# Performance work log

Measured on AMD Instinct MI355X. Metric: run time of the kernel, lower is better.

The kernel has to match this reference:

```python
import jax, jax.numpy as jnp
import numpy as np

N_LEVELS = 20
F = 2                      # n_features_per_level
LOG2T = 19
T = 1 << LOG2T             # hashmap size per level
BASE_RES = 16
PER_LEVEL_SCALE = 1.39
N_POINTS = 1_000_000

# 8 corner offsets of a voxel, (8, 3)
OFFSETS = np.array([[i, j, k] for i in (0, 1) for j in (0, 1) for k in (0, 1)], dtype=np.int32)
# spatial hash primes (only 3 needed for 3D input); uint32 multiply wraps like torch int32 bits
PRIME_Y = np.uint32(2654435761)
PRIME_Z = np.uint32(805459861)


def setup_inputs() -> dict:
    key = jax.random.key(0)
    k1, k2 = jax.random.split(key)
    x = jax.random.uniform(k1, (N_POINTS, 3), dtype=jnp.float32)  # points in [0,1)^3
    # nn.init.uniform_(weight, a=-1e-4, b=1e-4), one table per level, stacked
    tables = jax.random.uniform(k2, (N_LEVELS, T, F), minval=-1e-4, maxval=1e-4, dtype=jnp.float32)
    return {"x": x, "tables": tables}


def _hash(coords):
    # coords: (..., 3) int32 voxel corner indices -> (...,) int32 in [0, T)
    c = coords.astype(jnp.uint32)
    h = c[..., 0] ^ (c[..., 1] * PRIME_Y) ^ (c[..., 2] * PRIME_Z)
    return (h & jnp.uint32(T - 1)).astype(jnp.int32)


def _encode_level(x, table, resolution):
    xs = x * resolution                      # (B, 3)
    vmin = jnp.floor(xs).astype(jnp.int32)   # (B, 3)
    corners = vmin[:, None, :] + OFFSETS[None, :, :]   # (B, 8, 3)
    idx = _hash(corners)                     # (B, 8)
    e = table[idx]                           # (B, 8, F) gather
    w = xs - vmin                            # fractional position, (B, 3)
    wx, wy, wz = w[:, 0:1], w[:, 1:2], w[:, 2:3]
    # trilinear interpolation, exact lerp chain from the torch module
    c00 = e[:, 0] * (1 - wx) + e[:, 4] * wx
    c01 = e[:, 1] * (1 - wx) + e[:, 5] * wx
    c10 = e[:, 2] * (1 - wx) + e[:, 6] * wx
    c11 = e[:, 3] * (1 - wx) + e[:, 7] * wx
    c0 = c00 * (1 - wy) + c10 * wy
    c1 = c01 * (1 - wy) + c11 * wy
    return c0 * (1 - wz) + c1 * wz           # (B, F)


def reference(x, tables):
    outs = [_encode_level(x, tables[i], int(BASE_RES * PER_LEVEL_SCALE ** i))
            for i in range(N_LEVELS)]
    return jnp.concatenate(outs, axis=-1)    # (B, N_LEVELS * F) = (B, 40)
```

## Files before the change

kernel.cpp:

```cpp
#include <hip/hip_runtime.h>
#include <hip/hip_fp16.h>

#define NLEV 20
#define TSIZE (1u << 19)
#define TMASK (TSIZE - 1u)
#define PRIME_Y 2654435761u
#define PRIME_Z 805459861u

typedef float f32x2 __attribute__((ext_vector_type(2)));
typedef float f32x4 __attribute__((ext_vector_type(4)));

__device__ __constant__ int kRes[NLEV] = {
    16, 22, 30, 42, 59, 83, 115, 160, 222, 309,
    430, 598, 832, 1156, 1608, 2235, 3107, 4318, 6003, 8344};

__device__ __forceinline__ float2 encode_one(const float2* __restrict__ tbl,
                                             float r, float px, float py,
                                             float pz) {
  const float xs0 = px * r, xs1 = py * r, xs2 = pz * r;
  const float f0 = floorf(xs0), f1 = floorf(xs1), f2 = floorf(xs2);
  const float wx = xs0 - f0, wy = xs1 - f1, wz = xs2 - f2;
  const unsigned v0 = (unsigned)(int)f0;
  const unsigned v1 = (unsigned)(int)f1;
  const unsigned v2 = (unsigned)(int)f2;

  const unsigned hy0 = v1 * PRIME_Y, hy1 = (v1 + 1u) * PRIME_Y;
  const unsigned hz0 = v2 * PRIME_Z, hz1 = (v2 + 1u) * PRIME_Z;
  unsigned H[4];
  H[0] = hy0 ^ hz0;
  H[1] = hy0 ^ hz1;
  H[2] = hy1 ^ hz0;
  H[3] = hy1 ^ hz1;

  float2 e0[4], e1[4];

  if ((v0 & 1u) == 0u) {
#pragma unroll
    for (int j = 0; j < 4; ++j) {
      const unsigned i0 = (v0 ^ H[j]) & TMASK;
      const f32x4 q = *(const f32x4*)((const float*)tbl + 2u * (i0 & ~1u));
      const bool lo = (i0 & 1u) == 0u;
      e0[j] = lo ? make_float2(q.x, q.y) : make_float2(q.z, q.w);
      e1[j] = lo ? make_float2(q.z, q.w) : make_float2(q.x, q.y);
    }
  } else {
#pragma unroll
    for (int j = 0; j < 4; ++j) {
      e0[j] = tbl[(v0 ^ H[j]) & TMASK];
      e1[j] = tbl[((v0 + 1u) ^ H[j]) & TMASK];
    }
  }

  const float owx = 1.0f - wx, owy = 1.0f - wy, owz = 1.0f - wz;

  const float c00a = e0[0].x * owx + e1[0].x * wx;
  const float c01a = e0[1].x * owx + e1[1].x * wx;
  const float c10a = e0[2].x * owx + e1[2].x * wx;
  const float c11a = e0[3].x * owx + e1[3].x * wx;
  const float c0a = c00a * owy + c10a * wy;
  const float c1a = c01a * owy + c11a * wy;

  const float c00b = e0[0].y * owx + e1[0].y * wx;
  const float c01b = e0[1].y * owx + e1[1].y * wx;
  const float c10b = e0[2].y * owx + e1[2].y * wx;
  const float c11b = e0[3].y * owx + e1[3].y * wx;
  const float c0b = c00b * owy + c10b * wy;
  const float c1b = c01b * owy + c11b * wy;

  return make_float2(c0a * owz + c1a * wz, c0b * owz + c1b * wz);
}

__global__ __launch_bounds__(256) void enc_level_kernel(
    const float* __restrict__ x, const float* __restrict__ tables,
    unsigned* __restrict__ ws16, int n) {
  const int l = blockIdx.y;
  const int p = blockIdx.x * 256 + threadIdx.x;
  if (p >= n) return;
  const float px = __builtin_nontemporal_load(x + 3 * p + 0);
  const float py = __builtin_nontemporal_load(x + 3 * p + 1);
  const float pz = __builtin_nontemporal_load(x + 3 * p + 2);
  const float2* __restrict__ tbl = (const float2*)tables + (size_t)l * TSIZE;
  const float2 v = encode_one(tbl, (float)kRes[l], px, py, pz);
  const __half2 h = __floats2half2_rn(v.x, v.y);
  __builtin_nontemporal_store(*(const unsigned*)&h, ws16 + (size_t)l * n + p);
}

__global__ __launch_bounds__(256) void transpose_kernel(
    const unsigned* __restrict__ ws16, float* __restrict__ out, int n) {
  __shared__ unsigned lds[128 * 21];
  const int p0 = blockIdx.x * 128;
  const int t = threadIdx.x;
  const int npts = min(128, n - p0);

#pragma unroll
  for (int k = 0; k < 10; ++k) {
    const int g = t + k * 256;
    const int l = g >> 7;
    const int pl = g & 127;
    if (pl < npts) {
      lds[pl * 21 + l] =
          __builtin_nontemporal_load(ws16 + (size_t)l * n + p0 + pl);
    }
  }
  __syncthreads();

  f32x4* __restrict__ dst = (f32x4*)(out + (size_t)p0 * (NLEV * 2));
#pragma unroll
  for (int k = 0; k < 5; ++k) {
    const int g = t + k * 256;
    const int pl = g / 10;
    const int comp = g - pl * 10;
    if (pl < npts) {
      const unsigned u0 = lds[pl * 21 + comp * 2 + 0];
      const unsigned u1 = lds[pl * 21 + comp * 2 + 1];
      const float2 a = __half22float2(*(const __half2*)&u0);
      const float2 b = __half22float2(*(const __half2*)&u1);
      f32x4 v;
      v.x = a.x;
      v.y = a.y;
      v.z = b.x;
      v.w = b.y;
      __builtin_nontemporal_store(v, dst + g);
    }
  }
}

__global__ __launch_bounds__(256) void hash_enc_kernel(
    const float* __restrict__ x, const float* __restrict__ tables,
    float* __restrict__ out, int n) {
  int p = blockIdx.x * 256 + threadIdx.x;
  if (p >= n) return;
  const float px = x[3 * p + 0];
  const float py = x[3 * p + 1];
  const float pz = x[3 * p + 2];
  float o[NLEV * 2];
#pragma unroll
  for (int l = 0; l < NLEV; ++l) {
    const float2* tbl = (const float2*)tables + (size_t)l * TSIZE;
    const float2 v = encode_one(tbl, (float)kRes[l], px, py, pz);
    o[2 * l + 0] = v.x;
    o[2 * l + 1] = v.y;
  }
  float4* __restrict__ dst = (float4*)(out + (size_t)p * (NLEV * 2));
#pragma unroll
  for (int k = 0; k < 10; ++k) {
    dst[k] = make_float4(o[4 * k + 0], o[4 * k + 1], o[4 * k + 2], o[4 * k + 3]);
  }
}

extern "C" void kernel_launch(void* const* d_in, const int* in_sizes, int n_in,
                              void* d_out, int out_size, void* d_ws, size_t ws_size,
                              hipStream_t stream) {
  const float* x = (const float*)d_in[0];
  const float* tables = (const float*)d_in[1];
  float* out = (float*)d_out;
  const int n = in_sizes[0] / 3;
  const size_t ws_needed = (size_t)NLEV * n * sizeof(unsigned);

  if (ws_size >= ws_needed) {
    const int pblocks = (n + 255) / 256;
    dim3 grid1(pblocks, NLEV);
    enc_level_kernel<<<grid1, 256, 0, stream>>>(x, tables, (unsigned*)d_ws, n);
    const int tblocks = (n + 127) / 128;
    transpose_kernel<<<tblocks, 256, 0, stream>>>((const unsigned*)d_ws, out, n);
  } else {
    const int grid = (n + 255) / 256;
    hash_enc_kernel<<<grid, 256, 0, stream>>>(x, tables, out, n);
  }
}
```

Baseline: 653.7 us.

## Fuse fine hash-grid levels into a per-point kernel, keep coarse levels staged

Coarse levels 0-9 still run as a per-level grid that writes fp16 results to a workspace, which a smaller transpose kernel then scatters into the output. Fine levels 10-19 are computed by a new per-point kernel that loops over those levels and writes fp32 results directly into the upper half of each output row. This cuts workspace traffic and transpose work in half. The trade-off is that gathers across the large fine tables are interleaved per point rather than done one table at a time, which may reduce cache locality.

```diff
diff --git a/kernel.cpp b/kernel.cpp
--- a/kernel.cpp
+++ b/kernel.cpp
@@ -85,20 +85,51 @@
   __builtin_nontemporal_store(*(const unsigned*)&h, ws16 + (size_t)l * n + p);
 }
 
+__global__ __launch_bounds__(256) void fused_fine_kernel(
+    const float* __restrict__ x, const float* __restrict__ tables,
+    float* __restrict__ out, int n) {
+  const int p = blockIdx.x * 256 + threadIdx.x;
+  if (p >= n) return;
+  const float px = __builtin_nontemporal_load(x + 3 * p + 0);
+  const float py = __builtin_nontemporal_load(x + 3 * p + 1);
+  const float pz = __builtin_nontemporal_load(x + 3 * p + 2);
+
+  float o[20];
+#pragma unroll
+  for (int li = 0; li < 10; ++li) {
+    const int l = 10 + li;
+    const float2* __restrict__ tbl = (const float2*)tables + (size_t)l * TSIZE;
+    const float2 v = encode_one(tbl, (float)kRes[l], px, py, pz);
+    o[2 * li + 0] = v.x;
+    o[2 * li + 1] = v.y;
+  }
+
+  float* __restrict__ dstf = out + (size_t)p * (NLEV * 2) + 20;
+#pragma unroll
+  for (int k = 0; k < 5; ++k) {
+    f32x4 v;
+    v.x = o[4 * k + 0];
+    v.y = o[4 * k + 1];
+    v.z = o[4 * k + 2];
+    v.w = o[4 * k + 3];
+    __builtin_nontemporal_store(v, (f32x4*)(dstf + 4 * k));
+  }
+}
+
 __global__ __launch_bounds__(256) void transpose_kernel(
     const unsigned* __restrict__ ws16, float* __restrict__ out, int n) {
-  __shared__ unsigned lds[128 * 21];
+  __shared__ unsigned lds[128 * 11];
   const int p0 = blockIdx.x * 128;
   const int t = threadIdx.x;
   const int npts = min(128, n - p0);
 
 #pragma unroll
-  for (int k = 0; k < 10; ++k) {
+  for (int k = 0; k < 5; ++k) {
     const int g = t + k * 256;
     const int l = g >> 7;
     const int pl = g & 127;
     if (pl < npts) {
-      lds[pl * 21 + l] =
+      lds[pl * 11 + l] =
           __builtin_nontemporal_load(ws16 + (size_t)l * n + p0 + pl);
     }
   }
@@ -106,13 +137,13 @@
 
   f32x4* __restrict__ dst = (f32x4*)(out + (size_t)p0 * (NLEV * 2));
 #pragma unroll
-  for (int k = 0; k < 5; ++k) {
+  for (int k = 0; k < 3; ++k) {
     const int g = t + k * 256;
-    const int pl = g / 10;
-    const int comp = g - pl * 10;
-    if (pl < npts) {
-      const unsigned u0 = lds[pl * 21 + comp * 2 + 0];
-      const unsigned u1 = lds[pl * 21 + comp * 2 + 1];
+    const int pl = g / 5;
+    const int comp = g - pl * 5;
+    if (g < npts * 5) {
+      const unsigned u0 = lds[pl * 11 + comp * 2 + 0];
+      const unsigned u1 = lds[pl * 11 + comp * 2 + 1];
       const float2 a = __half22float2(*(const __half2*)&u0);
       const float2 b = __half22float2(*(const __half2*)&u1);
       f32x4 v;
@@ -120,7 +151,7 @@
       v.y = a.y;
       v.z = b.x;
       v.w = b.y;
-      __builtin_nontemporal_store(v, dst + g);
+      __builtin_nontemporal_store(v, dst + pl * 10 + comp);
     }
   }
 }
@@ -155,12 +186,13 @@
   const float* tables = (const float*)d_in[1];
   float* out = (float*)d_out;
   const int n = in_sizes[0] / 3;
-  const size_t ws_needed = (size_t)NLEV * n * sizeof(unsigned);
+  const size_t ws_needed = (size_t)10 * n * sizeof(unsigned);
 
   if (ws_size >= ws_needed) {
     const int pblocks = (n + 255) / 256;
-    dim3 grid1(pblocks, NLEV);
+    dim3 grid1(pblocks, 10);
     enc_level_kernel<<<grid1, 256, 0, stream>>>(x, tables, (unsigned*)d_ws, n);
+    fused_fine_kernel<<<pblocks, 256, 0, stream>>>(x, tables, out, n);
     const int tblocks = (n + 127) / 128;
     transpose_kernel<<<tblocks, 256, 0, stream>>>((const unsigned*)d_ws, out, n);
   } else {
```

Result: slower. 957.9 us (+46.5%).

## Fuse level encoding and output write into one cooperative grid-synced kernel

Applied to the files above, without the earlier changes.

Adds a cooperative kernel where each block keeps 1024 points in registers and processes levels in groups of four, with grid-wide syncs between groups. This keeps every block on the same four hash tables at once so the table working set stays cache-resident. Results are staged through LDS and written straight to the output, removing the fp16 workspace round trip and the separate transpose kernel. The cost is four grid barriers, occupancy limited to 4 blocks per CU, and partial-row strided output stores.

```diff
diff --git a/kernel.cpp b/kernel.cpp
--- a/kernel.cpp
+++ b/kernel.cpp
@@ -1,5 +1,8 @@
 #include <hip/hip_runtime.h>
 #include <hip/hip_fp16.h>
+#include <hip/hip_cooperative_groups.h>
+
+namespace cg = cooperative_groups;
 
 #define NLEV 20
 #define TSIZE (1u << 19)
@@ -68,6 +71,78 @@
   const float c1b = c01b * owy + c11b * wy;
 
   return make_float2(c0a * owz + c1a * wz, c0b * owz + c1b * wz);
+}
+
+__global__ __launch_bounds__(256, 4) void coop_fused_kernel(
+    const float* __restrict__ x, const float* __restrict__ tables,
+    float* __restrict__ out, int n) {
+  __shared__ float lds[256 * 9];
+  const int t = threadIdx.x;
+  const int base = blockIdx.x * 1024;
+  cg::grid_group grid = cg::this_grid();
+
+  float pcx[4], pcy[4], pcz[4];
+#pragma unroll
+  for (int i = 0; i < 4; ++i) {
+    const int p = base + t + 256 * i;
+    if (p < n) {
+      pcx[i] = __builtin_nontemporal_load(x + 3 * p + 0);
+      pcy[i] = __builtin_nontemporal_load(x + 3 * p + 1);
+      pcz[i] = __builtin_nontemporal_load(x + 3 * p + 2);
+    } else {
+      pcx[i] = 0.0f;
+      pcy[i] = 0.0f;
+      pcz[i] = 0.0f;
+    }
+  }
+
+  for (int g = 0; g < 5; ++g) {
+    float2 o[4][4];
+
+#pragma unroll
+    for (int j = 0; j < 4; ++j) {
+      const int l = 4 * g + j;
+      const float r = (float)kRes[l];
+      const float2* __restrict__ tbl = (const float2*)tables + (size_t)l * TSIZE;
+#pragma unroll
+      for (int i = 0; i < 4; ++i) {
+        const int p = base + t + 256 * i;
+        o[i][j] = (p < n) ? encode_one(tbl, r, pcx[i], pcy[i], pcz[i])
+                          : make_float2(0.0f, 0.0f);
+      }
+    }
+
+#pragma unroll
+    for (int i = 0; i < 4; ++i) {
+      __syncthreads();
+#pragma unroll
+      for (int j = 0; j < 4; ++j) {
+        lds[t * 9 + 2 * j + 0] = o[i][j].x;
+        lds[t * 9 + 2 * j + 1] = o[i][j].y;
+      }
+      __syncthreads();
+      const int cb = base + 256 * i;
+#pragma unroll
+      for (int k = 0; k < 2; ++k) {
+        const int g2 = t + k * 256;
+        const int pl = g2 >> 1;
+        const int comp = g2 & 1;
+        const int p = cb + pl;
+        if (p < n) {
+          const float* s = &lds[pl * 9 + comp * 4];
+          f32x4 v;
+          v.x = s[0];
+          v.y = s[1];
+          v.z = s[2];
+          v.w = s[3];
+          __builtin_nontemporal_store(
+              v, (f32x4*)(out + (size_t)p * (NLEV * 2) + 8 * g + 4 * comp));
+        }
+      }
+    }
+
+    if (g < 4) grid.sync();
+  }
 }
 
 __global__ __launch_bounds__(256) void enc_level_kernel(
@@ -155,8 +230,16 @@
   const float* tables = (const float*)d_in[1];
   float* out = (float*)d_out;
   const int n = in_sizes[0] / 3;
+
+  if (n <= 1024 * 1024) {
+    void* args[] = {(void*)&x, (void*)&tables, (void*)&out, (void*)&n};
+    hipError_t e = hipLaunchCooperativeKernel(
+        (const void*)coop_fused_kernel, dim3(1024), dim3(256), args, 0, stream);
+    if (e == hipSuccess) return;
+    (void)hipGetLastError();
+  }
+
   const size_t ws_needed = (size_t)NLEV * n * sizeof(unsigned);
-
   if (ws_size >= ws_needed) {
     const int pblocks = (n + 255) / 256;
     dim3 grid1(pblocks, NLEV);
```

Result: slower. 1.491 ms (+128.0%).
